# Optimization experiments

Measured on AMD Instinct MI355X. Metric: run time of the kernel, lower is better.

## Reference

```python
import jax, jax.numpy as jnp
import numpy as np

NUM_EDGE_TYPES = 4
TIME_STEPS = (1, 1)  # one propagation step per layer, 2 layers
HIDDEN = 128
N_NODES = 50000
N_EDGES = 400000


def setup_inputs() -> dict:
    key = jax.random.key(0)
    ks = jax.random.split(key, 8)
    states = jax.random.normal(ks[0], (N_NODES, HIDDEN), jnp.float32)
    etype = jax.random.randint(ks[1], (N_EDGES,), 0, NUM_EDGE_TYPES, jnp.int32)
    src = jax.random.randint(ks[2], (N_EDGES,), 0, N_NODES, jnp.int32)
    dst = jax.random.randint(ks[3], (N_EDGES,), 0, N_NODES, jnp.int32)
    edges = jnp.stack([etype, src, dst], axis=-1)  # [E, 3] = (type, src, dst)
    L = len(TIME_STEPS)
    std = HIDDEN ** -0.5  # matches tf.random_normal_initializer(stddev=H**-0.5)
    type_W = jax.random.normal(ks[4], (L, NUM_EDGE_TYPES, HIDDEN, HIDDEN), jnp.float32) * std
    type_b = jax.random.normal(ks[5], (L, NUM_EDGE_TYPES, HIDDEN), jnp.float32) * std
    gru_kernel = jax.random.normal(ks[6], (L, HIDDEN, 3 * HIDDEN), jnp.float32) * std
    gru_rkernel = jax.random.normal(ks[7], (L, HIDDEN, 3 * HIDDEN), jnp.float32) * std
    gru_bias = jnp.zeros((L, 2, 3 * HIDDEN), jnp.float32)  # [input_bias, recurrent_bias]
    return dict(states=states, edges=edges, type_W=type_W, type_b=type_b,
                gru_kernel=gru_kernel, gru_rkernel=gru_rkernel, gru_bias=gru_bias)


def _gru_cell(x, h, kernel, rkernel, bias):
    # tf.keras.layers.GRUCell with defaults (reset_after=True, sigmoid/tanh)
    mx = x @ kernel + bias[0]   # [N, 3H]
    mh = h @ rkernel + bias[1]  # [N, 3H]
    xz, xr, xh = jnp.split(mx, 3, axis=-1)
    hz, hr, hh = jnp.split(mh, 3, axis=-1)
    z = jax.nn.sigmoid(xz + hz)
    r = jax.nn.sigmoid(xr + hr)
    c = jnp.tanh(xh + r * hh)
    return z * h + (1.0 - z) * c


def _propagate(h, layer_no, edges, type_W, type_b):
    etype, src, dst = edges[:, 0], edges[:, 1], edges[:, 2]
    src_states = h[src]  # [E, H] irregular gather
    msgs = jnp.zeros_like(src_states)
    # per-edge-type dense transform, combined via masking (jit-friendly
    # equivalent of tf.dynamic_partition + per-type matmul)
    for t in range(NUM_EDGE_TYPES):
        mt = src_states @ type_W[layer_no, t] + type_b[layer_no, t]
        msgs = msgs + jnp.where((etype == t)[:, None], mt, 0.0)
    # scatter-add messages into destination nodes
    return jax.ops.segment_sum(msgs, dst, num_segments=h.shape[0])


def reference(states, edges, type_W, type_b, gru_kernel, gru_rkernel, gru_bias):
    h = states
    for layer_no, steps in enumerate(TIME_STEPS):
        for _ in range(steps):
            agg = _propagate(h, layer_no, edges, type_W, type_b)
            h = _gru_cell(agg, h, gru_kernel[layer_no], gru_rkernel[layer_no], gru_bias[layer_no])
    return h
```

## Files before the change

### kernel.cpp

```cpp
#include <hip/hip_runtime.h>
#include <hip/hip_bf16.h>

#define H 128
#define NT 4
#define CAP4 40

typedef __attribute__((ext_vector_type(8))) _Float16 half8;
typedef __attribute__((ext_vector_type(8))) unsigned short ushort8;
typedef __attribute__((ext_vector_type(4))) float f32x4;

#if defined(__has_builtin)
#if __has_builtin(__builtin_amdgcn_global_load_lds)
#define HAS_GLL 1
#endif
#endif
#ifndef HAS_GLL
#define HAS_GLL 0
#endif

__device__ __forceinline__ float bf2f(unsigned short u) {
    union { unsigned int i; float f; } v;
    v.i = ((unsigned int)u) << 16;
    return v.f;
}

__device__ __forceinline__ unsigned short f2bf(float f) {
    union { float f; unsigned int i; } v;
    v.f = f;
    unsigned int x = v.i;
    unsigned int r = (x + 0x7fffu + ((x >> 16) & 1u)) >> 16;
    return (unsigned short)r;
}

__device__ __forceinline__ float fsigmoid(float x) {
    return 1.0f / (1.0f + __expf(-x));
}
__device__ __forceinline__ float ftanh(float x) {
    return 1.0f - 2.0f / (__expf(2.0f * x) + 1.0f);
}

__device__ __forceinline__ float readf(const void* p, long i, int isbf) {
    return isbf ? bf2f(((const unsigned short*)p)[i]) : ((const float*)p)[i];
}

__device__ __forceinline__ void gll16(const _Float16* g, _Float16* l) {
#if HAS_GLL
    __builtin_amdgcn_global_load_lds(
        (const __attribute__((address_space(1))) unsigned int*)g,
        (__attribute__((address_space(3))) unsigned int*)l, 16, 0, 0);
#endif
}

__device__ __forceinline__ void stage64(
    const _Float16* __restrict__ gbase, int rstride, int row0, int kof,
    int maxrow, _Float16* lds) {
    const int wave = threadIdx.x >> 6, lane = threadIdx.x & 63;
#pragma unroll
    for (int s = 0; s < 2; s++) {
        int R = wave * 16 + s * 8;
        int rl = R + (lane >> 3);
        int rg = row0 + rl;
        if (rg >= maxrow) rg = maxrow - 1;
        int chunk = (lane & 7) ^ (rl & 7);
        const _Float16* gp = gbase + (size_t)rg * rstride + kof + chunk * 8;
#if HAS_GLL
        gll16(gp, lds + R * 64);
#else
        *(half8*)&lds[rl * 64 + (lane & 7) * 8] = *(const half8*)gp;
#endif
    }
}

__device__ __forceinline__ half8 frag(const _Float16* lds, int r, int g) {
    return *(const half8*)&lds[r * 64 + ((g ^ (r & 7)) * 8)];
}

__global__ void detect_dtype(const unsigned short* __restrict__ states_u16,
                             int* __restrict__ flag) {
    __shared__ int cnt;
    if (threadIdx.x == 0) cnt = 0;
    __syncthreads();
    int local = 0;
    for (int i = threadIdx.x; i < 1024; i += 256) {
        unsigned short u = states_u16[2 * i];
        int e = (u >> 7) & 0xFF;
        if (e >= 96 && e <= 158) local++;
    }
    atomicAdd(&cnt, local);
    __syncthreads();
    if (threadIdx.x == 0) *flag = (cnt >= 512) ? 1 : 0;
}

__global__ void prep_all(
    const void* __restrict__ states, const void* __restrict__ type_W,
    const void* __restrict__ type_b, const void* __restrict__ gk,
    const void* __restrict__ gr, const void* __restrict__ grub,
    _Float16* __restrict__ h16, _Float16* __restrict__ BTw,
    _Float16* __restrict__ BTg, float* __restrict__ btab,
    float* __restrict__ gbsum, float* __restrict__ gb0c,
    float* __restrict__ gb1c, int* __restrict__ counts4,
    const int* __restrict__ flag,
    long NNH, int nBTw, int nBTg, int NC4, int LAYERS) {
    long i = (long)blockIdx.x * 256 + threadIdx.x;
    const int fl = *flag;
    if (i < NNH) {
        h16[i] = (_Float16)readf(states, i, fl);
        return;
    }
    i -= NNH;
    if (i < nBTw) {
        int l = (int)(i >> 16);
        int r16 = (int)(i & 65535);
        int cblk = r16 >> 13;
        int rem = r16 & 8191;
        int g = rem >> 7;
        int mm = (rem >> 3) & 15;
        int j = rem & 7;
        int c = cblk * 16 + mm;
        int k = g * 8 + j;
        int t = k >> 7, kk = k & 127;
        BTw[i] = (_Float16)readf(type_W, (((long)(l * NT + t) * H) + kk) * H + c, fl);
        return;
    }
    i -= nBTw;
    if (i < nBTg) {
        int l = (int)(i >> 17);
        int r17 = (int)(i & 131071);
        int ncblk = r17 >> 12;
        int rem = r17 & 4095;
        int g = rem >> 7;
        int mm = (rem >> 3) & 15;
        int j = rem & 7;
        int nc = ncblk * 16 + mm;
        int k = g * 8 + j;
        int gblk = nc >> 6, gate = (nc >> 4) & 3;
        int c = gblk * 16 + (nc & 15);
        float v = 0.0f;
        if (gate == 0) {
            v = (k < 128) ? readf(gk, ((long)l * H + k) * 384 + c, fl)
                          : readf(gr, ((long)l * H + (k - 128)) * 384 + c, fl);
        } else if (gate == 1) {
            v = (k < 128) ? readf(gk, ((long)l * H + k) * 384 + 128 + c, fl)
                          : readf(gr, ((long)l * H + (k - 128)) * 384 + 128 + c, fl);
        } else if (gate == 2) {
            if (k < 128) v = readf(gk, ((long)l * H + k) * 384 + 256 + c, fl);
        } else {
            if (k >= 128) v = readf(gr, ((long)l * H + (k - 128)) * 384 + 256 + c, fl);
        }
        BTg[i] = (_Float16)v;
        return;
    }
    i -= nBTg;
    if (i < NC4) {
        counts4[i] = 0;
        return;
    }
    i -= NC4;
    {
        int j = (int)i;
        if (j < LAYERS * NT * H) btab[j] = readf(type_b, j, fl);
        if (j < LAYERS * 256) {
            int l = j >> 8, c = j & 255;
            gbsum[j] = readf(grub, (long)l * 768 + c, fl) +
                       readf(grub, (long)l * 768 + 384 + c, fl);
        }
        if (j < LAYERS * H) {
            int l = j >> 7, c = j & 127;
            gb0c[j] = readf(grub, (long)l * 768 + 256 + c, fl);
            gb1c[j] = readf(grub, (long)l * 768 + 384 + 256 + c, fl);
        }
    }
}

__global__ void place_edges4(const int* __restrict__ edges, int* __restrict__ counts4,
                             int* __restrict__ buckets4, int NE) {
    int e = blockIdx.x * 256 + threadIdx.x;
    if (e >= NE) return;
    int t = edges[3 * e], src = edges[3 * e + 1], dst = edges[3 * e + 2];
    int slot = atomicAdd(&counts4[dst * 4 + t], 1);
    if (slot < CAP4) buckets4[((size_t)dst * 4 + t) * CAP4 + slot] = src;
}

__global__ __launch_bounds__(256) void gather4(
    const _Float16* __restrict__ h16, const int* __restrict__ counts4,
    const int* __restrict__ buckets4, _Float16* __restrict__ A4, int NN) {
    int node = blockIdx.x * 4 + (threadIdx.x >> 6);
    int lane = threadIdx.x & 63;
    int q = lane >> 4, i = lane & 15;
    if (node >= NN) return;
    int cnt = counts4[node * 4 + q];
    if (cnt > CAP4) cnt = CAP4;
    const int* bkt = buckets4 + ((size_t)node * 4 + q) * CAP4;

    float acc[8] = {};
    int e = 0;
    for (; e + 4 <= cnt; e += 4) {
        int s0 = bkt[e], s1 = bkt[e + 1], s2 = bkt[e + 2], s3 = bkt[e + 3];
        half8 v0 = *(const half8*)&h16[(size_t)s0 * H + i * 8];
        half8 v1 = *(const half8*)&h16[(size_t)s1 * H + i * 8];
        half8 v2 = *(const half8*)&h16[(size_t)s2 * H + i * 8];
        half8 v3 = *(const half8*)&h16[(size_t)s3 * H + i * 8];
#pragma unroll
        for (int j = 0; j < 8; j++)
            acc[j] += ((float)v0[j] + (float)v1[j]) + ((float)v2[j] + (float)v3[j]);
    }
    if (e + 2 <= cnt) {
        int s0 = bkt[e], s1 = bkt[e + 1];
        half8 v0 = *(const half8*)&h16[(size_t)s0 * H + i * 8];
        half8 v1 = *(const half8*)&h16[(size_t)s1 * H + i * 8];
#pragma unroll
        for (int j = 0; j < 8; j++) acc[j] += (float)v0[j] + (float)v1[j];
        e += 2;
    }
    if (e < cnt) {
        int s0 = bkt[e];
        half8 v0 = *(const half8*)&h16[(size_t)s0 * H + i * 8];
#pragma unroll
        for (int j = 0; j < 8; j++) acc[j] += (float)v0[j];
    }

    half8 o;
#pragma unroll
    for (int j = 0; j < 8; j++) o[j] = (_Float16)acc[j];
    *(half8*)&A4[((size_t)node * 4 + q) * H + i * 8] = o;
}

__global__ __launch_bounds__(256, 3) void layer_fused(
    const _Float16* __restrict__ A4,
    const _Float16* __restrict__ h16,
    const _Float16* __restrict__ BTw,
    const _Float16* __restrict__ BTg,
    const float* __restrict__ btab,
    const int4* __restrict__ cnt4,
    const float* __restrict__ gbsum,
    const float* __restrict__ gb0c,
    const float* __restrict__ gb1c,
    _Float16* __restrict__ hnext,
    void* __restrict__ outbuf,
    const int* __restrict__ flag, int NN) {
    __shared__ __align__(16) _Float16 Asd[8192];
    __shared__ _Float16 hL[8192];
    __shared__ _Float16 aggL[8192];

    const int row0 = blockIdx.x * 64;
    const int tid = threadIdx.x;
    const int wave = tid >> 6, lane = tid & 63;
    const int m = lane & 15, quad = lane >> 4;
    const int wr = (wave & 1) * 32, wc = (wave >> 1) * 64;

    f32x4 acc[2][4] = {};

    stage64(A4, 512, row0, 0, NN, Asd);
    __syncthreads();
    for (int kc = 0; kc < 8; kc++) {
        const _Float16* cur = Asd + (kc & 1) * 4096;
        if (kc < 7) stage64(A4, 512, row0, (kc + 1) * 64, NN,
                            Asd + ((kc + 1) & 1) * 4096);
#pragma unroll
        for (int ks = 0; ks < 2; ks++) {
            const int gk = kc * 8 + ks * 4 + quad;
            half8 a[2], b[4];
#pragma unroll
            for (int mt = 0; mt < 2; mt++)
                a[mt] = frag(cur, wr + mt * 16 + m, ks * 4 + quad);
#pragma unroll
            for (int nt = 0; nt < 4; nt++)
                b[nt] = *(const half8*)&BTw[(((size_t)((wc >> 4) + nt)) << 13) +
                                            gk * 128 + m * 8];
#pragma unroll
            for (int mt = 0; mt < 2; mt++)
#pragma unroll
                for (int nt = 0; nt < 4; nt++)
                    acc[mt][nt] = __builtin_amdgcn_mfma_f32_16x16x32_f16(
                        a[mt], b[nt], acc[mt][nt], 0, 0, 0);
        }
        __syncthreads();
    }

    stage64(h16, H, row0, 0, NN, hL);
    stage64(h16, H, row0, 64, NN, hL + 4096);

#pragma unroll
    for (int mt = 0; mt < 2; mt++) {
#pragma unroll
        for (int i = 0; i < 4; i++) {
            int rl = wr + mt * 16 + quad * 4 + i;
            int rg = row0 + rl;
            if (rg >= NN) rg = NN - 1;
            int4 c4 = cnt4[rg];
#pragma unroll
            for (int nt = 0; nt < 4; nt++) {
                int c = wc + nt * 16 + m;
                float bias = c4.x * btab[c] + c4.y * btab[128 + c] +
                             c4.z * btab[256 + c] + c4.w * btab[384 + c];
                int tile = c >> 6, cc = c & 63, g = cc >> 3;
                aggL[tile * 4096 + rl * 64 + ((g ^ (rl & 7)) * 8) + (cc & 7)] =
                    (_Float16)(acc[mt][nt][i] + bias);
            }
        }
    }
    __syncthreads();
    _Float16* hout16 = Asd;

    const int fl = outbuf ? *flag : 0;
    for (int y = 0; y < 4; y++) {
        f32x4 p[2][4] = {};
#pragma unroll
        for (int kc = 0; kc < 4; kc++) {
            const int ntA = (kc < 2) ? 2 : 3;
            const _Float16* Asrc = (kc < 2) ? (aggL + kc * 4096)
                                            : (hL + (kc - 2) * 4096);
#pragma unroll
            for (int ks = 0; ks < 2; ks++) {
                const int gk = kc * 8 + ks * 4 + quad;
                half8 a[2], b3[3];
#pragma unroll
                for (int mt = 0; mt < 2; mt++)
                    a[mt] = frag(Asrc, wr + mt * 16 + m, ks * 4 + quad);
                const int ncb = y * 8 + (wc >> 4);
                b3[0] = *(const half8*)&BTg[(((size_t)(ncb + 0)) << 12) +
                                            gk * 128 + m * 8];
                b3[1] = *(const half8*)&BTg[(((size_t)(ncb + 1)) << 12) +
                                            gk * 128 + m * 8];
                b3[2] = *(const half8*)&BTg[(((size_t)(ncb + ntA)) << 12) +
                                            gk * 128 + m * 8];
#pragma unroll
                for (int mt = 0; mt < 2; mt++) {
                    p[mt][0] = __builtin_amdgcn_mfma_f32_16x16x32_f16(
                        a[mt], b3[0], p[mt][0], 0, 0, 0);
                    p[mt][1] = __builtin_amdgcn_mfma_f32_16x16x32_f16(
                        a[mt], b3[1], p[mt][1], 0, 0, 0);
                    p[mt][ntA] = __builtin_amdgcn_mfma_f32_16x16x32_f16(
                        a[mt], b3[2], p[mt][ntA], 0, 0, 0);
                }
            }
        }

        const int g8 = y * 2 + (wc >> 6);
        const int c = g8 * 16 + m;
        const float bz = gbsum[c];
        const float br = gbsum[128 + c];
        const float bx = gb0c[c];
        const float bh = gb1c[c];
        const int hsub = c >> 6, hcc = c & 63, hg = hcc >> 3, hj = hcc & 7;
#pragma unroll
        for (int mt = 0; mt < 2; mt++) {
#pragma unroll
            for (int i = 0; i < 4; i++) {
                int rl = wr + mt * 16 + quad * 4 + i;
                int row = row0 + rl;
                float z = fsigmoid(p[mt][0][i] + bz);
                float r = fsigmoid(p[mt][1][i] + br);
                float ccand =
                    ftanh((p[mt][2][i] + bx) + r * (p[mt][3][i] + bh));
                float hv = (float)hL[hsub * 4096 + rl * 64 +
                                     ((hg ^ (rl & 7)) * 8) + hj];
                float hn = z * hv + (1.0f - z) * ccand;
                if (outbuf) {
                    if (row < NN) {
                        size_t oi = (size_t)row * H + c;
                        if (fl) ((unsigned short*)outbuf)[oi] = f2bf(hn);
                        else    ((float*)outbuf)[oi] = hn;
                    }
                } else {
                    hout16[rl * 128 + c] = (_Float16)hn;
                }
            }
        }
    }

    if (!outbuf) {
        __syncthreads();
        int r = tid >> 2, s = tid & 3;
        int row = row0 + r;
        if (row < NN) {
            half8 v0 = *(const half8*)&hout16[r * 128 + s * 32];
            half8 v1 = *(const half8*)&hout16[r * 128 + s * 32 + 8];
            half8 v2 = *(const half8*)&hout16[r * 128 + s * 32 + 16];
            half8 v3 = *(const half8*)&hout16[r * 128 + s * 32 + 24];
            size_t o = (size_t)row * H + s * 32;
            *(half8*)&hnext[o] = v0;
            *(half8*)&hnext[o + 8] = v1;
            *(half8*)&hnext[o + 16] = v2;
            *(half8*)&hnext[o + 24] = v3;
        }
    }
}

extern "C" void kernel_launch(void* const* d_in, const int* in_sizes, int n_in,
                              void* d_out, int out_size, void* d_ws, size_t ws_size,
                              hipStream_t stream) {
    const void* states = d_in[0];
    const int*  edges  = (const int*)d_in[1];
    const void* type_W = d_in[2];
    const void* type_b = d_in[3];
    const void* gruk   = d_in[4];
    const void* grur   = d_in[5];
    const void* grub   = d_in[6];

    const int NN = in_sizes[0] / H;
    const int NE = in_sizes[1] / 3;
    const int nW = in_sizes[2];
    const int LAYERS = nW / (NT * H * H);

    char* w = (char*)d_ws;
    int* flag = (int*)w;                               w += 64;
    _Float16* h16A  = (_Float16*)w;                    w += (size_t)NN * H * 2;
    _Float16* h16B  = (_Float16*)w;                    w += (size_t)NN * H * 2;
    _Float16* A4    = (_Float16*)w;                    w += (size_t)NN * 4 * H * 2;
    _Float16* BTw = (_Float16*)w;                      w += (size_t)LAYERS * H * 512 * 2;
    _Float16* BTg = (_Float16*)w;                      w += (size_t)LAYERS * 512 * 256 * 2;
    float* btab  = (float*)w;                          w += (size_t)LAYERS * NT * H * 4;
    float* gbsum = (float*)w;                          w += (size_t)LAYERS * 256 * 4;
    float* gb0c  = (float*)w;                          w += (size_t)LAYERS * H * 4;
    float* gb1c  = (float*)w;                          w += (size_t)LAYERS * H * 4;
    int* counts4 = (int*)w;                            w += (size_t)NN * 4 * 4;
    int* buckets4 = (int*)w;

    detect_dtype<<<1, 256, 0, stream>>>((const unsigned short*)states, flag);

    const long NNH = (long)NN * H;
    const int nBTw = LAYERS * 65536;
    const int nBTg = LAYERS * 131072;
    const int NC4 = NN * 4;
    const long ptotal = NNH + nBTw + nBTg + NC4 + LAYERS * NT * H;
    prep_all<<<(int)((ptotal + 255) / 256), 256, 0, stream>>>(
        states, type_W, type_b, gruk, grur, grub,
        h16A, BTw, BTg, btab, gbsum, gb0c, gb1c, counts4, flag,
        NNH, nBTw, nBTg, NC4, LAYERS);

    place_edges4<<<(NE + 255) / 256, 256, 0, stream>>>(edges, counts4, buckets4, NE);

    const int rt64 = (NN + 63) / 64;
    for (int L = 0; L < LAYERS; L++) {
        const _Float16* hcur = (L & 1) ? h16B : h16A;
        _Float16* hnext      = (L & 1) ? h16A : h16B;

        gather4<<<(NN + 3) / 4, 256, 0, stream>>>(hcur, counts4, buckets4, A4, NN);

        layer_fused<<<rt64, 256, 0, stream>>>(
            A4, hcur,
            BTw + (size_t)L * H * 512,
            BTg + (size_t)L * 512 * 256,
            btab + (size_t)L * NT * H, (const int4*)counts4,
            gbsum + (size_t)L * 256, gb0c + (size_t)L * H, gb1c + (size_t)L * H,
            hnext, (L == LAYERS - 1) ? d_out : nullptr, flag, NN);
    }
}
```

Measured before the change: 297.8 us.

## Shrink layer_fused row tile to 32 and stage type weights in LDS

The fused layer kernel now processes 32 rows per block instead of 64, doubling the grid and raising the occupancy target to 4 blocks per CU. The first GEMM's weight tile is staged into LDS with global_load_lds each k-chunk instead of every wave reading it from global. The A-tile double buffering is removed in favour of a single buffer with two barriers per chunk. The GRU phase is split so each wave owns a column slice, and the output staging buffer is padded to stride 136 to reduce bank conflicts. The risk is lost load/compute overlap and more total weight traffic, since every block re-reads the weights for half as many rows.

```diff
diff --git a/kernel.cpp b/kernel.cpp
--- a/kernel.cpp
+++ b/kernel.cpp
@@ -48,27 +48,10 @@
     __builtin_amdgcn_global_load_lds(
         (const __attribute__((address_space(1))) unsigned int*)g,
         (__attribute__((address_space(3))) unsigned int*)l, 16, 0, 0);
+#else
+    const int lane = threadIdx.x & 63;
+    *(half8*)&l[lane * 8] = *(const half8*)g;
 #endif
-}
-
-__device__ __forceinline__ void stage64(
-    const _Float16* __restrict__ gbase, int rstride, int row0, int kof,
-    int maxrow, _Float16* lds) {
-    const int wave = threadIdx.x >> 6, lane = threadIdx.x & 63;
-#pragma unroll
-    for (int s = 0; s < 2; s++) {
-        int R = wave * 16 + s * 8;
-        int rl = R + (lane >> 3);
-        int rg = row0 + rl;
-        if (rg >= maxrow) rg = maxrow - 1;
-        int chunk = (lane & 7) ^ (rl & 7);
-        const _Float16* gp = gbase + (size_t)rg * rstride + kof + chunk * 8;
-#if HAS_GLL
-        gll16(gp, lds + R * 64);
-#else
-        *(half8*)&lds[rl * 64 + (lane & 7) * 8] = *(const half8*)gp;
-#endif
-    }
 }
 
 __device__ __forceinline__ half8 frag(const _Float16* lds, int r, int g) {
@@ -225,7 +208,7 @@
     *(half8*)&A4[((size_t)node * 4 + q) * H + i * 8] = o;
 }
 
-__global__ __launch_bounds__(256, 3) void layer_fused(
+__global__ __launch_bounds__(256, 4) void layer_fused(
     const _Float16* __restrict__ A4,
     const _Float16* __restrict__ h16,
     const _Float16* __restrict__ BTw,
@@ -238,122 +221,134 @@
     _Float16* __restrict__ hnext,
     void* __restrict__ outbuf,
     const int* __restrict__ flag, int NN) {
-    __shared__ __align__(16) _Float16 Asd[8192];
-    __shared__ _Float16 hL[8192];
-    __shared__ _Float16 aggL[8192];
-
-    const int row0 = blockIdx.x * 64;
+    __shared__ __align__(16) _Float16 As[2048];
+    __shared__ __align__(16) _Float16 Bs[8192];
+    __shared__ __align__(16) _Float16 aggL[4096];
+    __shared__ __align__(16) _Float16 hL[4096];
+
+    const int row0 = blockIdx.x * 32;
     const int tid = threadIdx.x;
     const int wave = tid >> 6, lane = tid & 63;
     const int m = lane & 15, quad = lane >> 4;
-    const int wr = (wave & 1) * 32, wc = (wave >> 1) * 64;
-
-    f32x4 acc[2][4] = {};
-
-    stage64(A4, 512, row0, 0, NN, Asd);
-    __syncthreads();
+
+    f32x4 acc[2][2] = {};
     for (int kc = 0; kc < 8; kc++) {
-        const _Float16* cur = Asd + (kc & 1) * 4096;
-        if (kc < 7) stage64(A4, 512, row0, (kc + 1) * 64, NN,
-                            Asd + ((kc + 1) & 1) * 4096);
+        __syncthreads();
+        {
+            int R = wave * 8;
+            int rl = R + (lane >> 3);
+            int rg = row0 + rl;
+            if (rg >= NN) rg = NN - 1;
+            int chunk = (lane & 7) ^ (rl & 7);
+            gll16(A4 + (size_t)rg * 512 + kc * 64 + chunk * 8, As + R * 64);
+        }
+#pragma unroll
+        for (int r = 0; r < 4; r++) {
+            int u = r * 256 + tid;
+            int cblk = u >> 7, gp = (u >> 4) & 7, mm = u & 15;
+            gll16(BTw + cblk * 8192 + (kc * 8 + gp) * 128 + mm * 8,
+                  Bs + (r * 256 + wave * 64) * 8);
+        }
+        __syncthreads();
 #pragma unroll
         for (int ks = 0; ks < 2; ks++) {
-            const int gk = kc * 8 + ks * 4 + quad;
-            half8 a[2], b[4];
+            half8 a[2], b[2];
 #pragma unroll
             for (int mt = 0; mt < 2; mt++)
-                a[mt] = frag(cur, wr + mt * 16 + m, ks * 4 + quad);
-#pragma unroll
-            for (int nt = 0; nt < 4; nt++)
-                b[nt] = *(const half8*)&BTw[(((size_t)((wc >> 4) + nt)) << 13) +
-                                            gk * 128 + m * 8];
+                a[mt] = frag(As, mt * 16 + m, ks * 4 + quad);
+#pragma unroll
+            for (int nt = 0; nt < 2; nt++)
+                b[nt] = *(const half8*)&Bs[(wave * 2 + nt) * 1024 +
+                                           (ks * 4 + quad) * 128 + m * 8];
 #pragma unroll
             for (int mt = 0; mt < 2; mt++)
 #pragma unroll
-                for (int nt = 0; nt < 4; nt++)
+                for (int nt = 0; nt < 2; nt++)
                     acc[mt][nt] = __builtin_amdgcn_mfma_f32_16x16x32_f16(
                         a[mt], b[nt], acc[mt][nt], 0, 0, 0);
         }
-        __syncthreads();
-    }
-
-    stage64(h16, H, row0, 0, NN, hL);
-    stage64(h16, H, row0, 64, NN, hL + 4096);
+    }
+
+    {
+        int R = wave * 8;
+        int rl = R + (lane >> 3);
+        int rg = row0 + rl;
+        if (rg >= NN) rg = NN - 1;
+        int chunk = (lane & 7) ^ (rl & 7);
+        gll16(h16 + (size_t)rg * H + chunk * 8, hL + R * 64);
+        gll16(h16 + (size_t)rg * H + 64 + chunk * 8, hL + 2048 + R * 64);
+    }
 
 #pragma unroll
     for (int mt = 0; mt < 2; mt++) {
 #pragma unroll
         for (int i = 0; i < 4; i++) {
-            int rl = wr + mt * 16 + quad * 4 + i;
+            int rl = mt * 16 + quad * 4 + i;
             int rg = row0 + rl;
             if (rg >= NN) rg = NN - 1;
             int4 c4 = cnt4[rg];
 #pragma unroll
-            for (int nt = 0; nt < 4; nt++) {
-                int c = wc + nt * 16 + m;
+            for (int nt = 0; nt < 2; nt++) {
+                int c = wave * 32 + nt * 16 + m;
                 float bias = c4.x * btab[c] + c4.y * btab[128 + c] +
                              c4.z * btab[256 + c] + c4.w * btab[384 + c];
-                int tile = c >> 6, cc = c & 63, g = cc >> 3;
-                aggL[tile * 4096 + rl * 64 + ((g ^ (rl & 7)) * 8) + (cc & 7)] =
+                int sub = c >> 6, cc = c & 63, g = cc >> 3;
+                aggL[sub * 2048 + rl * 64 + ((g ^ (rl & 7)) * 8) + (cc & 7)] =
                     (_Float16)(acc[mt][nt][i] + bias);
             }
         }
     }
     __syncthreads();
-    _Float16* hout16 = Asd;
-
+
+    _Float16* hout16 = Bs;
     const int fl = outbuf ? *flag : 0;
-    for (int y = 0; y < 4; y++) {
+    const int y = wave;
+#pragma unroll
+    for (int ch = 0; ch < 2; ch++) {
         f32x4 p[2][4] = {};
+        const int ncb0 = y * 8 + ch * 4;
 #pragma unroll
         for (int kc = 0; kc < 4; kc++) {
             const int ntA = (kc < 2) ? 2 : 3;
-            const _Float16* Asrc = (kc < 2) ? (aggL + kc * 4096)
-                                            : (hL + (kc - 2) * 4096);
+            const _Float16* Asrc = (kc < 2) ? (aggL + kc * 2048)
+                                            : (hL + (kc - 2) * 2048);
 #pragma unroll
             for (int ks = 0; ks < 2; ks++) {
                 const int gk = kc * 8 + ks * 4 + quad;
-                half8 a[2], b3[3];
-#pragma unroll
-                for (int mt = 0; mt < 2; mt++)
-                    a[mt] = frag(Asrc, wr + mt * 16 + m, ks * 4 + quad);
-                const int ncb = y * 8 + (wc >> 4);
-                b3[0] = *(const half8*)&BTg[(((size_t)(ncb + 0)) << 12) +
-                                            gk * 128 + m * 8];
-                b3[1] = *(const half8*)&BTg[(((size_t)(ncb + 1)) << 12) +
-                                            gk * 128 + m * 8];
-                b3[2] = *(const half8*)&BTg[(((size_t)(ncb + ntA)) << 12) +
-                                            gk * 128 + m * 8];
-#pragma unroll
-                for (int mt = 0; mt < 2; mt++) {
-                    p[mt][0] = __builtin_amdgcn_mfma_f32_16x16x32_f16(
-                        a[mt], b3[0], p[mt][0], 0, 0, 0);
-                    p[mt][1] = __builtin_amdgcn_mfma_f32_16x16x32_f16(
-                        a[mt], b3[1], p[mt][1], 0, 0, 0);
-                    p[mt][ntA] = __builtin_amdgcn_mfma_f32_16x16x32_f16(
-                        a[mt], b3[2], p[mt][ntA], 0, 0, 0);
-                }
+                half8 a0 = frag(Asrc, m, ks * 4 + quad);
+                half8 a1 = frag(Asrc, 16 + m, ks * 4 + quad);
+                half8 b0 = *(const half8*)&BTg[(size_t)(ncb0 + 0) * 4096 +
+                                               gk * 128 + m * 8];
+                half8 b1 = *(const half8*)&BTg[(size_t)(ncb0 + 1) * 4096 +
+                                               gk * 128 + m * 8];
+                half8 b2 = *(const half8*)&BTg[(size_t)(ncb0 + ntA) * 4096 +
+                                               gk * 128 + m * 8];
+                p[0][0] = __builtin_amdgcn_mfma_f32_16x16x32_f16(a0, b0, p[0][0], 0, 0, 0);
+                p[1][0] = __builtin_amdgcn_mfma_f32_16x16x32_f16(a1, b0, p[1][0], 0, 0, 0);
+                p[0][1] = __builtin_amdgcn_mfma_f32_16x16x32_f16(a0, b1, p[0][1], 0, 0, 0);
+                p[1][1] = __builtin_amdgcn_mfma_f32_16x16x32_f16(a1, b1, p[1][1], 0, 0, 0);
+                p[0][ntA] = __builtin_amdgcn_mfma_f32_16x16x32_f16(a0, b2, p[0][ntA], 0, 0, 0);
+                p[1][ntA] = __builtin_amdgcn_mfma_f32_16x16x32_f16(a1, b2, p[1][ntA], 0, 0, 0);
             }
         }
 
-        const int g8 = y * 2 + (wc >> 6);
-        const int c = g8 * 16 + m;
+        const int c = (2 * y + ch) * 16 + m;
         const float bz = gbsum[c];
         const float br = gbsum[128 + c];
         const float bx = gb0c[c];
         const float bh = gb1c[c];
-        const int hsub = c >> 6, hcc = c & 63, hg = hcc >> 3, hj = hcc & 7;
+        const int sub = c >> 6, cc = c & 63, hg = cc >> 3, hj = cc & 7;
 #pragma unroll
         for (int mt = 0; mt < 2; mt++) {
 #pragma unroll
             for (int i = 0; i < 4; i++) {
-                int rl = wr + mt * 16 + quad * 4 + i;
+                int rl = mt * 16 + quad * 4 + i;
                 int row = row0 + rl;
                 float z = fsigmoid(p[mt][0][i] + bz);
                 float r = fsigmoid(p[mt][1][i] + br);
                 float ccand =
                     ftanh((p[mt][2][i] + bx) + r * (p[mt][3][i] + bh));
-                float hv = (float)hL[hsub * 4096 + rl * 64 +
+                float hv = (float)hL[sub * 2048 + rl * 64 +
                                      ((hg ^ (rl & 7)) * 8) + hj];
                 float hn = z * hv + (1.0f - z) * ccand;
                 if (outbuf) {
@@ -363,7 +358,7 @@
                         else    ((float*)outbuf)[oi] = hn;
                     }
                 } else {
-                    hout16[rl * 128 + c] = (_Float16)hn;
+                    hout16[rl * 136 + c] = (_Float16)hn;
                 }
             }
         }
@@ -371,18 +366,14 @@
 
     if (!outbuf) {
         __syncthreads();
-        int r = tid >> 2, s = tid & 3;
+        int r = tid >> 3, s = tid & 7;
         int row = row0 + r;
         if (row < NN) {
-            half8 v0 = *(const half8*)&hout16[r * 128 + s * 32];
-            half8 v1 = *(const half8*)&hout16[r * 128 + s * 32 + 8];
-            half8 v2 = *(const half8*)&hout16[r * 128 + s * 32 + 16];
-            half8 v3 = *(const half8*)&hout16[r * 128 + s * 32 + 24];
-            size_t o = (size_t)row * H + s * 32;
+            half8 v0 = *(const half8*)&hout16[r * 136 + s * 16];
+            half8 v1 = *(const half8*)&hout16[r * 136 + s * 16 + 8];
+            size_t o = (size_t)row * H + s * 16;
             *(half8*)&hnext[o] = v0;
             *(half8*)&hnext[o + 8] = v1;
-            *(half8*)&hnext[o + 16] = v2;
-            *(half8*)&hnext[o + 24] = v3;
         }
     }
 }
@@ -431,14 +422,14 @@
 
     place_edges4<<<(NE + 255) / 256, 256, 0, stream>>>(edges, counts4, buckets4, NE);
 
-    const int rt64 = (NN + 63) / 64;
+    const int rt32 = (NN + 31) / 32;
     for (int L = 0; L < LAYERS; L++) {
         const _Float16* hcur = (L & 1) ? h16B : h16A;
         _Float16* hnext      = (L & 1) ? h16A : h16B;
 
         gather4<<<(NN + 3) / 4, 256, 0, stream>>>(hcur, counts4, buckets4, A4, NN);
 
-        layer_fused<<<rt64, 256, 0, stream>>>(
+        layer_fused<<<rt32, 256, 0, stream>>>(
             A4, hcur,
             BTw + (size_t)L * H * 512,
             BTg + (size_t)L * 512 * 256,
```

Result: faster. 261.3 us (-12.3%).
